# Performance work log

Hardware: AMD Instinct MI355X
Metric: run time of the kernel (lower is better)

The kernel has to match this reference:

```python
import jax, jax.numpy as jnp
import numpy as np


def setup_inputs() -> dict:
    key = jax.random.key(0)
    B, n = 1048576, 8
    x = jax.random.normal(key, (B, n, n), dtype=jnp.float32)
    return {"x": x, "num_iters": 5}


def reference(x, num_iters):
    # FusedMHC.forward: flatten to [B, n, n] in fp32, run Sinkhorn, cast back.
    input_dtype = x.dtype
    n = x.shape[-1]
    M = jnp.exp(x.reshape(-1, n, n).astype(jnp.float32))  # positive kernel matrix
    # num_iters alternating row / column normalizations (Sinkhorn-Knopp)
    for _ in range(num_iters):
        M = M / jnp.sum(M, axis=-1, keepdims=True)  # row normalize
        M = M / jnp.sum(M, axis=-2, keepdims=True)  # col normalize
    return M.reshape(x.shape).astype(input_dtype)
```

## Files before the change

### kernel.cpp

```cpp
#include <hip/hip_runtime.h>


#define N 8

__global__ __launch_bounds__(256) void sinkhorn8_kernel(
    const float* __restrict__ x,
    float* __restrict__ out,
    const int* __restrict__ num_iters_p,
    int B)
{
    int b = blockIdx.x * blockDim.x + threadIdx.x;
    if (b >= B) return;

    const int num_iters = *num_iters_p;

    const float4* __restrict__ xv = (const float4*)(x + (size_t)b * (N * N));
    float4* __restrict__ ov = (float4*)(out + (size_t)b * (N * N));

    float M[N * N];

#pragma unroll
    for (int k = 0; k < 16; ++k) {
        float4 v = xv[k];
        M[4 * k + 0] = __expf(v.x);
        M[4 * k + 1] = __expf(v.y);
        M[4 * k + 2] = __expf(v.z);
        M[4 * k + 3] = __expf(v.w);
    }

    for (int it = 0; it < num_iters; ++it) {
#pragma unroll
        for (int r = 0; r < N; ++r) {
            float s = 0.f;
#pragma unroll
            for (int c = 0; c < N; ++c) s += M[r * N + c];
            float inv = __builtin_amdgcn_rcpf(s);
#pragma unroll
            for (int c = 0; c < N; ++c) M[r * N + c] *= inv;
        }
#pragma unroll
        for (int c = 0; c < N; ++c) {
            float s = 0.f;
#pragma unroll
            for (int r = 0; r < N; ++r) s += M[r * N + c];
            float inv = __builtin_amdgcn_rcpf(s);
#pragma unroll
            for (int r = 0; r < N; ++r) M[r * N + c] *= inv;
        }
    }

#pragma unroll
    for (int k = 0; k < 16; ++k) {
        float4 v;
        v.x = M[4 * k + 0];
        v.y = M[4 * k + 1];
        v.z = M[4 * k + 2];
        v.w = M[4 * k + 3];
        ov[k] = v;
    }
}

extern "C" void kernel_launch(void* const* d_in, const int* in_sizes, int n_in,
                              void* d_out, int out_size, void* d_ws, size_t ws_size,
                              hipStream_t stream) {
    const float* x = (const float*)d_in[0];
    const int* num_iters = (const int*)d_in[1];
    float* out = (float*)d_out;

    int B = in_sizes[0] / (N * N);
    int block = 256;
    int grid = (B + block - 1) / block;

    sinkhorn8_kernel<<<grid, block, 0, stream>>>(x, out, num_iters, B);
}
```

Baseline: 452.0 us.

## Distribute each 8x8 matrix over 16 lanes with shuffle reductions

Instead of one thread owning a whole 8x8 matrix in registers, 16 threads cooperate per matrix, each holding one float4 (half a row). Row sums use one xor-shuffle and column sums use three shuffle stages across lanes. This makes global loads and stores fully coalesced and cuts per-thread register use to raise occupancy, at the cost of cross-lane shuffle traffic in every iteration.

```diff
diff --git a/kernel.cpp b/kernel.cpp
--- a/kernel.cpp
+++ b/kernel.cpp
@@ -9,55 +9,43 @@
     const int* __restrict__ num_iters_p,
     int B)
 {
-    int b = blockIdx.x * blockDim.x + threadIdx.x;
-    if (b >= B) return;
+    int tid = blockIdx.x * blockDim.x + threadIdx.x;
+    int m = tid >> 4;
+    if (m >= B) return;
 
     const int num_iters = *num_iters_p;
 
-    const float4* __restrict__ xv = (const float4*)(x + (size_t)b * (N * N));
-    float4* __restrict__ ov = (float4*)(out + (size_t)b * (N * N));
+    float4 v = ((const float4*)x)[tid];
 
-    float M[N * N];
+    v.x = __expf(v.x);
+    v.y = __expf(v.y);
+    v.z = __expf(v.z);
+    v.w = __expf(v.w);
 
+    for (int it = 0; it < num_iters; ++it) {
+        float rs = v.x + v.y + v.z + v.w;
+        rs += __shfl_xor(rs, 1, 64);
+        float rinv = __builtin_amdgcn_rcpf(rs);
+        v.x *= rinv;
+        v.y *= rinv;
+        v.z *= rinv;
+        v.w *= rinv;
+
+        float4 cs = v;
 #pragma unroll
-    for (int k = 0; k < 16; ++k) {
-        float4 v = xv[k];
-        M[4 * k + 0] = __expf(v.x);
-        M[4 * k + 1] = __expf(v.y);
-        M[4 * k + 2] = __expf(v.z);
-        M[4 * k + 3] = __expf(v.w);
+        for (int d = 2; d <= 8; d <<= 1) {
+            cs.x += __shfl_xor(cs.x, d, 64);
+            cs.y += __shfl_xor(cs.y, d, 64);
+            cs.z += __shfl_xor(cs.z, d, 64);
+            cs.w += __shfl_xor(cs.w, d, 64);
+        }
+        v.x *= __builtin_amdgcn_rcpf(cs.x);
+        v.y *= __builtin_amdgcn_rcpf(cs.y);
+        v.z *= __builtin_amdgcn_rcpf(cs.z);
+        v.w *= __builtin_amdgcn_rcpf(cs.w);
     }
 
-    for (int it = 0; it < num_iters; ++it) {
-#pragma unroll
-        for (int r = 0; r < N; ++r) {
-            float s = 0.f;
-#pragma unroll
-            for (int c = 0; c < N; ++c) s += M[r * N + c];
-            float inv = __builtin_amdgcn_rcpf(s);
-#pragma unroll
-            for (int c = 0; c < N; ++c) M[r * N + c] *= inv;
-        }
-#pragma unroll
-        for (int c = 0; c < N; ++c) {
-            float s = 0.f;
-#pragma unroll
-            for (int r = 0; r < N; ++r) s += M[r * N + c];
-            float inv = __builtin_amdgcn_rcpf(s);
-#pragma unroll
-            for (int r = 0; r < N; ++r) M[r * N + c] *= inv;
-        }
-    }
-
-#pragma unroll
-    for (int k = 0; k < 16; ++k) {
-        float4 v;
-        v.x = M[4 * k + 0];
-        v.y = M[4 * k + 1];
-        v.z = M[4 * k + 2];
-        v.w = M[4 * k + 3];
-        ov[k] = v;
-    }
+    ((float4*)out)[tid] = v;
 }
 
 extern "C" void kernel_launch(void* const* d_in, const int* in_sizes, int n_in,
@@ -68,8 +56,9 @@
     float* out = (float*)d_out;
 
     int B = in_sizes[0] / (N * N);
+    long long total_threads = (long long)B * 16;
     int block = 256;
-    int grid = (B + block - 1) / block;
+    long long grid = (total_threads + block - 1) / block;
 
-    sinkhorn8_kernel<<<grid, block, 0, stream>>>(x, out, num_iters, B);
+    sinkhorn8_kernel<<<(int)grid, block, 0, stream>>>(x, out, num_iters, B);
 }
```

Result: slower. 482.8 us (+6.8%).

## Map one matrix row per lane and reduce columns with DPP cross-lane ops

Applied to the files above, without the earlier changes.

Each lane now holds two matrix rows (from two matrices) instead of one thread owning a whole 8x8 matrix. Column sums are done with three DPP xor shuffles across the 8 lanes holding a matrix's rows. This makes global loads coalesced across lanes instead of each thread striding 256 bytes, and cuts per-thread register use. Stores become nontemporal. It assumes B is divisible by 16, and the lane-to-row mapping and DPP control patterns must be exact for results to be correct.

```diff
diff --git a/kernel.cpp b/kernel.cpp
--- a/kernel.cpp
+++ b/kernel.cpp
@@ -3,61 +3,90 @@
 
 #define N 8
 
+typedef float f32x4 __attribute__((ext_vector_type(4)));
+
+template <int CTRL>
+__device__ __forceinline__ float dpp_xor(float x) {
+    int r = __builtin_amdgcn_update_dpp(0, __float_as_int(x), CTRL, 0xF, 0xF, true);
+    return __int_as_float(r);
+}
+
+__device__ __forceinline__ void load_exp(const f32x4* __restrict__ x4,
+                                         size_t idx, float* r) {
+    f32x4 v0 = x4[idx];
+    f32x4 v1 = x4[idx + 1];
+    r[0] = __expf(v0.x); r[1] = __expf(v0.y);
+    r[2] = __expf(v0.z); r[3] = __expf(v0.w);
+    r[4] = __expf(v1.x); r[5] = __expf(v1.y);
+    r[6] = __expf(v1.z); r[7] = __expf(v1.w);
+}
+
+__device__ __forceinline__ void row_norm(float* r) {
+    float s = ((r[0] + r[1]) + (r[2] + r[3])) + ((r[4] + r[5]) + (r[6] + r[7]));
+    float inv = __builtin_amdgcn_rcpf(s);
+#pragma unroll
+    for (int i = 0; i < 8; ++i) r[i] *= inv;
+}
+
+__device__ __forceinline__ void col_norm(float* r) {
+    float c[8];
+#pragma unroll
+    for (int i = 0; i < 8; ++i) c[i] = r[i];
+#pragma unroll
+    for (int i = 0; i < 8; ++i) c[i] += dpp_xor<0xB1>(c[i]);
+#pragma unroll
+    for (int i = 0; i < 8; ++i) c[i] += dpp_xor<0x4E>(c[i]);
+#pragma unroll
+    for (int i = 0; i < 8; ++i) c[i] += dpp_xor<0x128>(c[i]);
+#pragma unroll
+    for (int i = 0; i < 8; ++i) r[i] *= __builtin_amdgcn_rcpf(c[i]);
+}
+
+__device__ __forceinline__ void store_row(f32x4* __restrict__ o4,
+                                          size_t idx, const float* r) {
+    f32x4 v0 = {r[0], r[1], r[2], r[3]};
+    f32x4 v1 = {r[4], r[5], r[6], r[7]};
+    __builtin_nontemporal_store(v0, &o4[idx]);
+    __builtin_nontemporal_store(v1, &o4[idx + 1]);
+}
+
 __global__ __launch_bounds__(256) void sinkhorn8_kernel(
     const float* __restrict__ x,
     float* __restrict__ out,
     const int* __restrict__ num_iters_p,
-    int B)
+    int nwaves)
 {
-    int b = blockIdx.x * blockDim.x + threadIdx.x;
-    if (b >= B) return;
+    int T = blockIdx.x * blockDim.x + threadIdx.x;
+    int w = T >> 6;
+    if (w >= nwaves) return;
 
     const int num_iters = *num_iters_p;
 
-    const float4* __restrict__ xv = (const float4*)(x + (size_t)b * (N * N));
-    float4* __restrict__ ov = (float4*)(out + (size_t)b * (N * N));
+    int l = T & 63;
+    int g = l >> 4;
+    int t = l & 15;
+    int b = (t >> 2) & 1;
+    int row = (t & 3) | ((t >> 1) & 4);
 
-    float M[N * N];
+    size_t idxA = (size_t)w * 256 + (size_t)g * 32 + (size_t)b * 16 + (size_t)row * 2;
+    size_t idxB = idxA + 128;
 
-#pragma unroll
-    for (int k = 0; k < 16; ++k) {
-        float4 v = xv[k];
-        M[4 * k + 0] = __expf(v.x);
-        M[4 * k + 1] = __expf(v.y);
-        M[4 * k + 2] = __expf(v.z);
-        M[4 * k + 3] = __expf(v.w);
+    const f32x4* x4 = (const f32x4*)x;
+    f32x4* o4 = (f32x4*)out;
+
+    float A[8], Bv[8];
+    load_exp(x4, idxA, A);
+    load_exp(x4, idxB, Bv);
+
+    for (int it = 0; it < num_iters; ++it) {
+        row_norm(A);
+        row_norm(Bv);
+        col_norm(A);
+        col_norm(Bv);
     }
 
-    for (int it = 0; it < num_iters; ++it) {
-#pragma unroll
-        for (int r = 0; r < N; ++r) {
-            float s = 0.f;
-#pragma unroll
-            for (int c = 0; c < N; ++c) s += M[r * N + c];
-            float inv = __builtin_amdgcn_rcpf(s);
-#pragma unroll
-            for (int c = 0; c < N; ++c) M[r * N + c] *= inv;
-        }
-#pragma unroll
-        for (int c = 0; c < N; ++c) {
-            float s = 0.f;
-#pragma unroll
-            for (int r = 0; r < N; ++r) s += M[r * N + c];
-            float inv = __builtin_amdgcn_rcpf(s);
-#pragma unroll
-            for (int r = 0; r < N; ++r) M[r * N + c] *= inv;
-        }
-    }
-
-#pragma unroll
-    for (int k = 0; k < 16; ++k) {
-        float4 v;
-        v.x = M[4 * k + 0];
-        v.y = M[4 * k + 1];
-        v.z = M[4 * k + 2];
-        v.w = M[4 * k + 3];
-        ov[k] = v;
-    }
+    store_row(o4, idxA, A);
+    store_row(o4, idxB, Bv);
 }
 
 extern "C" void kernel_launch(void* const* d_in, const int* in_sizes, int n_in,
@@ -68,8 +97,10 @@
     float* out = (float*)d_out;
 
     int B = in_sizes[0] / (N * N);
+    int nwaves = B / 16;
+
+    long long threads = (long long)nwaves * 64;
     int block = 256;
-    int grid = (B + block - 1) / block;
-
-    sinkhorn8_kernel<<<grid, block, 0, stream>>>(x, out, num_iters, B);
+    long long grid = (threads + block - 1) / block;
+    sinkhorn8_kernel<<<(int)grid, block, 0, stream>>>(x, out, num_iters, nwaves);
 }
```

New measurement: 463.6 us. +2.6%, slower.

## Spread each 8x8 matrix across 8 lanes with DPP column reductions

Applied to the files above, without the earlier changes.

Each matrix is now split so that every lane holds one row (8 floats) and eight lanes together hold one matrix. Each lane works on four matrices, so one wave covers 32 matrices. Column sums are computed with DPP cross-lane butterfly adds instead of in per-thread registers. Loads become two adjacent float4 per row per lane, which should give better-coalesced memory access and much lower register pressure than 64 floats per thread, raising occupancy. A separate tail kernel handles leftover matrices, and the DPP steps add cross-lane work.

```diff
diff --git a/kernel.cpp b/kernel.cpp
--- a/kernel.cpp
+++ b/kernel.cpp
@@ -3,31 +3,113 @@
 
 #define N 8
 
+typedef float f32x4 __attribute__((ext_vector_type(4)));
+
+template <int CTRL>
+__device__ __forceinline__ float dpp_xor(float x) {
+    int r = __builtin_amdgcn_update_dpp(0, __float_as_int(x), CTRL, 0xF, 0xF, true);
+    return __int_as_float(r);
+}
+
+__device__ __forceinline__ void exp8(f32x4 v0, f32x4 v1, float* r) {
+    r[0] = __expf(v0.x); r[1] = __expf(v0.y);
+    r[2] = __expf(v0.z); r[3] = __expf(v0.w);
+    r[4] = __expf(v1.x); r[5] = __expf(v1.y);
+    r[6] = __expf(v1.z); r[7] = __expf(v1.w);
+}
+
+__device__ __forceinline__ void row_norm(float* r) {
+    float s = ((r[0] + r[1]) + (r[2] + r[3])) + ((r[4] + r[5]) + (r[6] + r[7]));
+    float inv = __builtin_amdgcn_rcpf(s);
+#pragma unroll
+    for (int i = 0; i < 8; ++i) r[i] *= inv;
+}
+
+__device__ __forceinline__ void col_norm(float* r) {
+#pragma unroll
+    for (int i = 0; i < 8; ++i) {
+        float c = r[i];
+        c += dpp_xor<0xB1>(c);
+        c += dpp_xor<0x4E>(c);
+        c += dpp_xor<0x128>(c);
+        r[i] *= __builtin_amdgcn_rcpf(c);
+    }
+}
+
+__device__ __forceinline__ void store8(f32x4* __restrict__ o4, size_t idx,
+                                       const float* r) {
+    f32x4 v0 = {r[0], r[1], r[2], r[3]};
+    f32x4 v1 = {r[4], r[5], r[6], r[7]};
+    o4[idx] = v0;
+    o4[idx + 1] = v1;
+}
+
 __global__ __launch_bounds__(256) void sinkhorn8_kernel(
     const float* __restrict__ x,
     float* __restrict__ out,
     const int* __restrict__ num_iters_p,
-    int B)
+    int nwaves)
 {
-    int b = blockIdx.x * blockDim.x + threadIdx.x;
-    if (b >= B) return;
+    int T = blockIdx.x * blockDim.x + threadIdx.x;
+    int w = T >> 6;
+    if (w >= nwaves) return;
 
     const int num_iters = *num_iters_p;
 
-    const float4* __restrict__ xv = (const float4*)(x + (size_t)b * (N * N));
-    float4* __restrict__ ov = (float4*)(out + (size_t)b * (N * N));
+    int l = T & 63;
+    int g = l >> 4;
+    int t = l & 15;
+    int b = (t >> 2) & 1;
+    int row = (t & 3) | ((t >> 1) & 4);
+
+    size_t base = (size_t)w * 512 + (size_t)g * 32 + (size_t)b * 16 + (size_t)row * 2;
+
+    const f32x4* x4 = (const f32x4*)x;
+    f32x4* o4 = (f32x4*)out;
+
+    f32x4 a0 = x4[base + 0],   a1 = x4[base + 1];
+    f32x4 b0 = x4[base + 128], b1 = x4[base + 129];
+    f32x4 c0 = x4[base + 256], c1 = x4[base + 257];
+    f32x4 d0 = x4[base + 384], d1 = x4[base + 385];
+
+    float A[8], Bv[8], C[8], D[8];
+    exp8(a0, a1, A);
+    exp8(b0, b1, Bv);
+    exp8(c0, c1, C);
+    exp8(d0, d1, D);
+
+    for (int it = 0; it < num_iters; ++it) {
+        row_norm(A); row_norm(Bv); row_norm(C); row_norm(D);
+        col_norm(A); col_norm(Bv); col_norm(C); col_norm(D);
+    }
+
+    store8(o4, base + 0, A);
+    store8(o4, base + 128, Bv);
+    store8(o4, base + 256, C);
+    store8(o4, base + 384, D);
+}
+
+__global__ __launch_bounds__(64) void sinkhorn8_tail(
+    const float* __restrict__ x,
+    float* __restrict__ out,
+    const int* __restrict__ num_iters_p,
+    int nfull, int B)
+{
+    int m = nfull + blockIdx.x * blockDim.x + threadIdx.x;
+    if (m >= B) return;
+    const int num_iters = *num_iters_p;
 
     float M[N * N];
-
+    const f32x4* xv = (const f32x4*)(x + (size_t)m * (N * N));
+    f32x4* ov = (f32x4*)(out + (size_t)m * (N * N));
 #pragma unroll
     for (int k = 0; k < 16; ++k) {
-        float4 v = xv[k];
+        f32x4 v = xv[k];
         M[4 * k + 0] = __expf(v.x);
         M[4 * k + 1] = __expf(v.y);
         M[4 * k + 2] = __expf(v.z);
         M[4 * k + 3] = __expf(v.w);
     }
-
     for (int it = 0; it < num_iters; ++it) {
 #pragma unroll
         for (int r = 0; r < N; ++r) {
@@ -48,14 +130,9 @@
             for (int r = 0; r < N; ++r) M[r * N + c] *= inv;
         }
     }
-
 #pragma unroll
     for (int k = 0; k < 16; ++k) {
-        float4 v;
-        v.x = M[4 * k + 0];
-        v.y = M[4 * k + 1];
-        v.z = M[4 * k + 2];
-        v.w = M[4 * k + 3];
+        f32x4 v = {M[4 * k], M[4 * k + 1], M[4 * k + 2], M[4 * k + 3]};
         ov[k] = v;
     }
 }
@@ -68,8 +145,17 @@
     float* out = (float*)d_out;
 
     int B = in_sizes[0] / (N * N);
-    int block = 256;
-    int grid = (B + block - 1) / block;
+    int nwaves = B / 32;
+    int nfull = nwaves * 32;
 
-    sinkhorn8_kernel<<<grid, block, 0, stream>>>(x, out, num_iters, B);
+    if (nwaves > 0) {
+        long long threads = (long long)nwaves * 64;
+        int block = 256;
+        long long grid = (threads + block - 1) / block;
+        sinkhorn8_kernel<<<(int)grid, block, 0, stream>>>(x, out, num_iters, nwaves);
+    }
+    int tail = B - nfull;
+    if (tail > 0) {
+        sinkhorn8_tail<<<1, 64, 0, stream>>>(x, out, num_iters, nfull, B);
+    }
 }
```

After: 435.2 us. -3.7%, faster.
